# Optimization experiments

Hardware: AMD Instinct MI355X
Metric: run time of the kernel (lower is better)

Reference implementation:

```python
import jax, jax.numpy as jnp
import numpy as np

EMBED_DIM = 1024
NUM_HEADS = 16
HEAD_DIM = EMBED_DIM // NUM_HEADS
SCALE = 1.0 / np.sqrt(HEAD_DIM).astype(np.float32)


def setup_inputs() -> dict:
    key = jax.random.key(0)
    ks = jax.random.split(key, 9)
    B, T, C = 2, 2048, EMBED_DIM
    s = 1.0 / np.sqrt(C).astype(np.float32)  # torch Linear init scale (approx, uniform bound)
    return {
        "x_q": jax.random.normal(ks[0], (B, T, C), dtype=jnp.float32),
        "attn_mask": jnp.zeros((T, T), dtype=jnp.float32),
        "Wq": jax.random.uniform(ks[1], (C, C), jnp.float32, -s, s),
        "bq": jax.random.uniform(ks[2], (C,), jnp.float32, -s, s),
        "Wk": jax.random.uniform(ks[3], (C, C), jnp.float32, -s, s),
        "bk": jax.random.uniform(ks[4], (C,), jnp.float32, -s, s),
        "Wv": jax.random.uniform(ks[5], (C, C), jnp.float32, -s, s),
        "bv": jax.random.uniform(ks[6], (C,), jnp.float32, -s, s),
        "Wo": jax.random.uniform(ks[7], (C, C), jnp.float32, -s, s),
        "bo": jax.random.uniform(ks[8], (C,), jnp.float32, -s, s),
    }


def reference(x_q, attn_mask, Wq, bq, Wk, bk, Wv, bv, Wo, bo):
    B, Tq, C = x_q.shape
    # self-attention: x_kv = x_q
    q = (x_q @ Wq.T + bq).reshape(B, Tq, NUM_HEADS, HEAD_DIM)
    k = (x_q @ Wk.T + bk).reshape(B, Tq, NUM_HEADS, HEAD_DIM)
    v = (x_q @ Wv.T + bv).reshape(B, Tq, NUM_HEADS, HEAD_DIM)
    # (B, H, Tq, Tk)
    scores = jnp.einsum('bqhd,bkhd->bhqk', q, k) * SCALE
    scores = scores + attn_mask[None, None, :, :]  # 2D additive mask path
    attn = jax.nn.softmax(scores, axis=-1)  # dropout p=0.0 -> identity
    out = jnp.einsum('bhqk,bkhd->bqhd', attn, v).reshape(B, Tq, C)
    out = out @ Wo.T + bo
    return out
```

## Files before the change

kernel.cpp:

```cpp
#include <hip/hip_runtime.h>
#include <hip/hip_bf16.h>
#include <stdint.h>

typedef _Float16 f16x8_t __attribute__((ext_vector_type(8)));
typedef _Float16 f16x4_t __attribute__((ext_vector_type(4)));
typedef float    f32x4_t __attribute__((ext_vector_type(4)));
typedef float    f32x16_t __attribute__((ext_vector_type(16)));

#define T_SEQ 2048
#define NH    16
#define HD    64
#define CDIM  1024
#define NTOK  4096
#define QSCALE 0.18033688011112042f
#define LOG2E  1.4426950408889634f

__device__ __forceinline__ void async_ld16(void* lds, const void* g) {
    __builtin_amdgcn_global_load_lds(
        (const __attribute__((address_space(1))) uint32_t*)g,
        (__attribute__((address_space(3))) uint32_t*)lds, 16, 0, 0);
}

__global__ __launch_bounds__(256)
void prep_all(const float* __restrict__ x, const float* __restrict__ Wq,
              const float* __restrict__ Wk, const float* __restrict__ Wv,
              const float* __restrict__ Wo, const float* __restrict__ mask,
              _Float16* __restrict__ xh, _Float16* __restrict__ Wqkvh,
              _Float16* __restrict__ Woh, int* __restrict__ flag)
{
    const int XQ = NTOK * CDIM / 4;
    const int WQ = CDIM * CDIM / 4;
    int i = blockIdx.x * 256 + threadIdx.x;
    if (i < XQ + 4 * WQ) {
        const float* s; _Float16* d; int off;
        if (i < XQ) { s = x; d = xh; off = i; }
        else {
            int j = i - XQ; int w = j >> 18; off = j & (WQ - 1);
            s = (w == 0) ? Wq : (w == 1) ? Wk : (w == 2) ? Wv : Wo;
            d = (w == 3) ? Woh : Wqkvh + (size_t)w * CDIM * CDIM;
        }
        float4 v = ((const float4*)s)[off];
        f16x4_t h = {(_Float16)v.x, (_Float16)v.y, (_Float16)v.z, (_Float16)v.w};
        ((f16x4_t*)d)[off] = h;
    } else {
        int off = i - (XQ + 4 * WQ);
        float4 v = ((const float4*)mask)[off];
        if (v.x != 0.f || v.y != 0.f || v.z != 0.f || v.w != 0.f) atomicOr(flag, 1);
    }
}

template<int MODE>
__global__ __launch_bounds__(256)
void gemm_f16(const _Float16* __restrict__ Ag, const _Float16* __restrict__ Bg,
              const float* __restrict__ b0, const float* __restrict__ b1,
              const float* __restrict__ b2,
              _Float16* __restrict__ Qo, _Float16* __restrict__ Ko,
              _Float16* __restrict__ Vto, float* __restrict__ Fo)
{
    __shared__ _Float16 sA[3][128 * 32];
    __shared__ _Float16 sB[3][128 * 32];
    const int K = CDIM;
    const int tid  = threadIdx.x;
    const int lane = tid & 63, wv = tid >> 6;
    const int wr = wv >> 1, wc = wv & 1;
    const int bid = blockIdx.x;
    const int xcd = bid & 7, L = bid >> 3;
    const int sb = L & 31, st = L >> 5;
    const int rowA0 = (st * 8 + (sb & 7)) * 128;
    const int rowB0 = (xcd * 4 + (sb >> 3)) * 128;
    const int srow = lane >> 2;
    const int scol = (lane & 3) * 8;
    const int fr = lane & 15, fg = lane >> 4;
    f32x4_t acc[4][4] = {};

#define STAGE(buf, kk) do {                                                     \
        _Pragma("unroll")                                                       \
        for (int i_ = 0; i_ < 2; ++i_) {                                        \
            const int eoff = i_ * 2048 + wv * 512;                              \
            const int r_ = i_ * 64 + wv * 16 + srow;                            \
            async_ld16(&sA[buf][eoff], Ag + (size_t)(rowA0 + r_) * K + (kk) + scol); \
            async_ld16(&sB[buf][eoff], Bg + (size_t)(rowB0 + r_) * K + (kk) + scol); \
        } } while (0)

    STAGE(0, 0);
    int cur = 0;
    for (int k0 = 0; k0 < K; k0 += 32) {
        const int nxt = (cur == 2) ? 0 : cur + 1;
        if (k0 + 32 < K) {
            STAGE(nxt, k0 + 32);
            asm volatile("s_waitcnt vmcnt(4)" ::: "memory");
        } else {
            asm volatile("s_waitcnt vmcnt(0)" ::: "memory");
        }
        __builtin_amdgcn_s_barrier();
        __builtin_amdgcn_sched_barrier(0);
        f16x8_t a[4], b[4];
#pragma unroll
        for (int mi = 0; mi < 4; ++mi)
            a[mi] = *(const f16x8_t*)&sA[cur][(wr * 64 + mi * 16 + fr) * 32 + fg * 8];
#pragma unroll
        for (int ni = 0; ni < 4; ++ni)
            b[ni] = *(const f16x8_t*)&sB[cur][(wc * 64 + ni * 16 + fr) * 32 + fg * 8];
#pragma unroll
        for (int mi = 0; mi < 4; ++mi)
#pragma unroll
            for (int ni = 0; ni < 4; ++ni)
                acc[mi][ni] = __builtin_amdgcn_mfma_f32_16x16x32_f16(a[mi], b[ni], acc[mi][ni], 0, 0, 0);
        cur = nxt;
    }
#undef STAGE

    if (MODE == 0) {
        const int which = rowA0 >> 10;
        const float* bp = (which == 0) ? b0 : ((which == 1) ? b1 : b2);
#pragma unroll
        for (int mi = 0; mi < 4; ++mi) {
            const int cc = (rowA0 & 1023) + wr * 64 + mi * 16 + fg * 4;
            const float4 bv = *(const float4*)&bp[cc];
            const int h = cc >> 6, d0 = cc & 63;
#pragma unroll
            for (int ni = 0; ni < 4; ++ni) {
                const int tok = rowB0 + wc * 64 + ni * 16 + fr;
                const int bh = (tok >> 11) * NH + h, tt = tok & (T_SEQ - 1);
                const float v0 = acc[mi][ni][0] + bv.x, v1 = acc[mi][ni][1] + bv.y;
                const float v2 = acc[mi][ni][2] + bv.z, v3 = acc[mi][ni][3] + bv.w;
                if (which == 0) {
                    f16x4_t hq = {(_Float16)(v0 * QSCALE), (_Float16)(v1 * QSCALE),
                                  (_Float16)(v2 * QSCALE), (_Float16)(v3 * QSCALE)};
                    *(f16x4_t*)&Qo[((size_t)bh * T_SEQ + tt) * HD + d0] = hq;
                } else if (which == 1) {
                    f16x4_t hk = {(_Float16)v0, (_Float16)v1, (_Float16)v2, (_Float16)v3};
                    *(f16x4_t*)&Ko[((size_t)bh * 32 + (tt >> 6)) * 4096 +
                                   (d0 >> 3) * 512 + (tt & 63) * 8 + (d0 & 7)] = hk;
                } else {
                    const size_t vb_ = ((size_t)bh * 32 + (tt >> 6)) * 4096 +
                                       (size_t)((tt >> 3) & 7) * 512 + (tt & 7);
                    Vto[vb_ + (d0 + 0) * 8] = (_Float16)v0;
                    Vto[vb_ + (d0 + 1) * 8] = (_Float16)v1;
                    Vto[vb_ + (d0 + 2) * 8] = (_Float16)v2;
                    Vto[vb_ + (d0 + 3) * 8] = (_Float16)v3;
                }
            }
        }
    } else {
#pragma unroll
        for (int mi = 0; mi < 4; ++mi) {
            const int cc = rowA0 + wr * 64 + mi * 16 + fg * 4;
            const float4 bv = *(const float4*)&b0[cc];
#pragma unroll
            for (int ni = 0; ni < 4; ++ni) {
                const int tok = rowB0 + wc * 64 + ni * 16 + fr;
                float4 ov = {acc[mi][ni][0] + bv.x, acc[mi][ni][1] + bv.y,
                             acc[mi][ni][2] + bv.z, acc[mi][ni][3] + bv.w};
                *(float4*)&Fo[(size_t)tok * CDIM + cc] = ov;
            }
        }
    }
}

__global__ __launch_bounds__(256, 2)
void attn_f16(const _Float16* __restrict__ Q, const _Float16* __restrict__ Kc,
              const _Float16* __restrict__ Vc, const float* __restrict__ mask,
              const int* __restrict__ mflag, _Float16* __restrict__ AO)
{
    __shared__ __align__(16) _Float16 sK[3][4096];
    __shared__ __align__(16) _Float16 sV[3][4096];

    const int tid = threadIdx.x;
    const int lane = tid & 63, wv = tid >> 6;
    const int ln = lane & 31, hi = lane >> 5;
    const int bid = blockIdx.x;
    const int xcd = bid & 7, idx = bid >> 3;
    const int bh = xcd * 4 + (idx & 3);
    const int qx = idx >> 2;
    const int b = bh >> 4, h = bh & (NH - 1);
    const int q0 = qx * 128 + wv * 32;
    const _Float16* Qb  = Q  + (size_t)bh * T_SEQ * HD;
    const _Float16* Kbh = Kc + (size_t)bh * (T_SEQ * HD);
    const _Float16* Vbh = Vc + (size_t)bh * (T_SEQ * HD);
    const int soff = tid * 8;

    f16x8_t qf[4];
#pragma unroll
    for (int dc = 0; dc < 4; ++dc)
        qf[dc] = *(const f16x8_t*)&Qb[(size_t)(q0 + ln) * HD + dc * 16 + hi * 8];

    f32x16_t o0 = {}, o1 = {};
    float m_run = -1e30f, l_run = 0.f;
    const int mf = mflag[0];

    async_ld16(&sK[0][soff],        Kbh + soff);
    async_ld16(&sK[0][2048 + soff], Kbh + 2048 + soff);
    async_ld16(&sV[0][soff],        Vbh + soff);
    async_ld16(&sV[0][2048 + soff], Vbh + 2048 + soff);
    int cur = 0;

    for (int t = 0; t < T_SEQ / 64; ++t) {
        const int nxt = (cur == 2) ? 0 : cur + 1;
        if (t + 1 < T_SEQ / 64) {
            const int goff = (t + 1) * 4096;
            async_ld16(&sK[nxt][soff],        Kbh + goff + soff);
            async_ld16(&sK[nxt][2048 + soff], Kbh + goff + 2048 + soff);
            async_ld16(&sV[nxt][soff],        Vbh + goff + soff);
            async_ld16(&sV[nxt][2048 + soff], Vbh + goff + 2048 + soff);
            asm volatile("s_waitcnt vmcnt(4)" ::: "memory");
        } else {
            asm volatile("s_waitcnt vmcnt(0)" ::: "memory");
        }
        __builtin_amdgcn_s_barrier();
        __builtin_amdgcn_sched_barrier(0);

        f32x16_t s0 = {}, s1 = {};
        __builtin_amdgcn_s_setprio(1);
#pragma unroll
        for (int dc = 0; dc < 4; ++dc) {
            f16x8_t kf0 = *(const f16x8_t*)&sK[cur][(2 * dc + hi) * 512 + ln * 8];
            f16x8_t kf1 = *(const f16x8_t*)&sK[cur][(2 * dc + hi) * 512 + (32 + ln) * 8];
            s0 = __builtin_amdgcn_mfma_f32_32x32x16_f16(kf0, qf[dc], s0, 0, 0, 0);
            s1 = __builtin_amdgcn_mfma_f32_32x32x16_f16(kf1, qf[dc], s1, 0, 0, 0);
        }
        __builtin_amdgcn_s_setprio(0);

        if (mf) {
            const float* mrow = mask + (size_t)(q0 + ln) * T_SEQ + t * 64;
#pragma unroll
            for (int r2 = 0; r2 < 16; ++r2) {
                const int row = (r2 & 3) + 8 * (r2 >> 2) + 4 * hi;
                s0[r2] += mrow[row] * LOG2E;
                s1[r2] += mrow[32 + row] * LOG2E;
            }
        }

        float mt[8];
#pragma unroll
        for (int i = 0; i < 8; ++i)
            mt[i] = fmaxf(fmaxf(s0[2 * i], s0[2 * i + 1]), fmaxf(s1[2 * i], s1[2 * i + 1]));
#pragma unroll
        for (int st = 4; st > 0; st >>= 1)
#pragma unroll
            for (int i = 0; i < st; ++i) mt[i] = fmaxf(mt[i], mt[i + st]);
        float tmax = fmaxf(mt[0], __shfl_xor(mt[0], 32, 64));

        if (!__all(tmax <= m_run + 8.0f)) {
            const float mnew = fmaxf(m_run, tmax);
            const float sc = __builtin_amdgcn_exp2f(m_run - mnew);
            m_run = mnew;
            l_run *= sc;
#pragma unroll
            for (int r2 = 0; r2 < 16; ++r2) {
                const int row = (r2 & 3) + 8 * (r2 >> 2) + 4 * hi;
                const float scr = __shfl(sc, row, 64);
                o0[r2] *= scr;
                o1[r2] *= scr;
            }
        }

#pragma unroll
        for (int r2 = 0; r2 < 16; ++r2) {
            s0[r2] = __builtin_amdgcn_exp2f(s0[r2] - m_run);
            s1[r2] = __builtin_amdgcn_exp2f(s1[r2] - m_run);
        }
        float sm[8];
#pragma unroll
        for (int i = 0; i < 8; ++i)
            sm[i] = (s0[2 * i] + s0[2 * i + 1]) + (s1[2 * i] + s1[2 * i + 1]);
#pragma unroll
        for (int st = 4; st > 0; st >>= 1)
#pragma unroll
            for (int i = 0; i < st; ++i) sm[i] += sm[i + st];
        l_run += sm[0] + __shfl_xor(sm[0], 32, 64);

        f16x8_t pa[4];
#pragma unroll
        for (int g = 0; g < 2; ++g) {
            const f32x16_t& sg = g ? s1 : s0;
            uint32_t W[8];
#pragma unroll
            for (int t2 = 0; t2 < 8; ++t2) {
                auto pk = __builtin_amdgcn_cvt_pkrtz(sg[2 * t2], sg[2 * t2 + 1]);
                W[t2] = __builtin_bit_cast(uint32_t, pk);
            }
#pragma unroll
            for (int c2 = 0; c2 < 2; ++c2) {
                uint32_t a0 = W[4 * c2 + 0], a1 = W[4 * c2 + 1];
                uint32_t a2 = W[4 * c2 + 2], a3 = W[4 * c2 + 3];
                asm("v_permlane32_swap_b32 %0, %1" : "+v"(a0), "+v"(a2));
                asm("v_permlane32_swap_b32 %0, %1" : "+v"(a1), "+v"(a3));
                union { uint32_t w[4]; f16x8_t v; } u;
                u.w[0] = a0; u.w[1] = a1; u.w[2] = a2; u.w[3] = a3;
                pa[g * 2 + c2] = u.v;
            }
        }

        __builtin_amdgcn_s_setprio(1);
#pragma unroll
        for (int c = 0; c < 4; ++c) {
            f16x8_t vb0 = *(const f16x8_t*)&sV[cur][(2 * c + hi) * 512 + ln * 8];
            f16x8_t vb1 = *(const f16x8_t*)&sV[cur][(2 * c + hi) * 512 + (32 + ln) * 8];
            o0 = __builtin_amdgcn_mfma_f32_32x32x16_f16(pa[c], vb0, o0, 0, 0, 0);
            o1 = __builtin_amdgcn_mfma_f32_32x32x16_f16(pa[c], vb1, o1, 0, 0, 0);
        }
        __builtin_amdgcn_s_setprio(0);
        cur = nxt;
    }

    const float linv = 1.f / l_run;
#pragma unroll
    for (int r2 = 0; r2 < 16; ++r2) {
        const int row = (r2 & 3) + 8 * (r2 >> 2) + 4 * hi;
        const float inv = __shfl(linv, row, 64);
        const size_t base = (size_t)(b * T_SEQ + q0 + row) * CDIM + h * HD;
        AO[base + ln]      = (_Float16)(o0[r2] * inv);
        AO[base + 32 + ln] = (_Float16)(o1[r2] * inv);
    }
}

extern "C" void kernel_launch(void* const* d_in, const int* in_sizes, int n_in,
                              void* d_out, int out_size, void* d_ws, size_t ws_size,
                              hipStream_t stream) {
    const float* x    = (const float*)d_in[0];
    const float* mask = (const float*)d_in[1];
    const float* Wq   = (const float*)d_in[2];
    const float* bq   = (const float*)d_in[3];
    const float* Wk   = (const float*)d_in[4];
    const float* bk   = (const float*)d_in[5];
    const float* Wv   = (const float*)d_in[6];
    const float* bv   = (const float*)d_in[7];
    const float* Wo   = (const float*)d_in[8];
    const float* bo   = (const float*)d_in[9];
    float* out = (float*)d_out;

    char* ws = (char*)d_ws;
    _Float16* xh    = (_Float16*)(ws);
    _Float16* Wqkvh = (_Float16*)(ws + (8u  << 20));
    _Float16* Woh   = (_Float16*)(ws + (14u << 20));
    _Float16* Qp    = (_Float16*)(ws + (16u << 20));
    _Float16* Kc    = (_Float16*)(ws + (24u << 20));
    _Float16* Vc    = (_Float16*)(ws + (32u << 20));
    int* mflag      = (int*)(ws + (40u << 20));
    _Float16* AO    = xh;

    hipMemsetAsync(mflag, 0, 4, stream);
    prep_all<<<12288, 256, 0, stream>>>(x, Wq, Wk, Wv, Wo, mask, xh, Wqkvh, Woh, mflag);
    gemm_f16<0><<<768, 256, 0, stream>>>(Wqkvh, xh, bq, bk, bv, Qp, Kc, Vc, nullptr);
    attn_f16<<<512, 256, 0, stream>>>(Qp, Kc, Vc, mask, mflag, AO);
    gemm_f16<1><<<256, 256, 0, stream>>>(Woh, AO, bo, nullptr, nullptr,
                                         nullptr, nullptr, nullptr, out);
}
```

Measured before the change: 128.9 us.

## Split attention KV range across two wave groups with LDS merge

The attention kernel now uses 512-thread blocks in which two 4-wave groups each process half of the key/value sequence for the same 128 query rows. Their online-softmax partial results are merged through shared memory at the end. Each group double-buffers its own K/V tiles and synchronises with __syncthreads, replacing the earlier triple-buffered waitcnt scheme. The aim is more waves per CU and shorter per-wave serial loops, at the cost of an extra merge step, block-wide barriers, and the larger LDS footprint limiting occupancy.

Measured after the change: 131.3 us. Within noise of the previous version (+1.8%).

```diff
diff --git a/kernel.cpp b/kernel.cpp
--- a/kernel.cpp
+++ b/kernel.cpp
@@ -158,27 +158,36 @@
     }
 }
 
-__global__ __launch_bounds__(256, 2)
+__global__ __launch_bounds__(512, 4)
 void attn_f16(const _Float16* __restrict__ Q, const _Float16* __restrict__ Kc,
               const _Float16* __restrict__ Vc, const float* __restrict__ mask,
               const int* __restrict__ mflag, _Float16* __restrict__ AO)
 {
-    __shared__ __align__(16) _Float16 sK[3][4096];
-    __shared__ __align__(16) _Float16 sV[3][4096];
+    __shared__ __align__(16) _Float16 smem[32768];
 
     const int tid = threadIdx.x;
     const int lane = tid & 63, wv = tid >> 6;
+    const int g = wv >> 2, wl = wv & 3;
     const int ln = lane & 31, hi = lane >> 5;
     const int bid = blockIdx.x;
-    const int xcd = bid & 7, idx = bid >> 3;
-    const int bh = xcd * 4 + (idx & 3);
-    const int qx = idx >> 2;
+    const int swz = (bid & 7) * 64 + (bid >> 3);
+    const int qx = swz & 15, bh = swz >> 4;
     const int b = bh >> 4, h = bh & (NH - 1);
-    const int q0 = qx * 128 + wv * 32;
+    const int q0 = qx * 128 + wl * 32;
     const _Float16* Qb  = Q  + (size_t)bh * T_SEQ * HD;
     const _Float16* Kbh = Kc + (size_t)bh * (T_SEQ * HD);
     const _Float16* Vbh = Vc + (size_t)bh * (T_SEQ * HD);
-    const int soff = tid * 8;
+    _Float16* pK = smem + g * 16384;
+    _Float16* pV = pK + 8192;
+    const int soff = (tid & 255) * 8;
+
+#define ASTAGE(buf, t) do {                                                   \
+        const int goff_ = (t) * 4096;                                         \
+        async_ld16(&pK[(buf) * 4096 + soff],        Kbh + goff_ + soff);        \
+        async_ld16(&pK[(buf) * 4096 + 2048 + soff], Kbh + goff_ + 2048 + soff); \
+        async_ld16(&pV[(buf) * 4096 + soff],        Vbh + goff_ + soff);        \
+        async_ld16(&pV[(buf) * 4096 + 2048 + soff], Vbh + goff_ + 2048 + soff); \
+    } while (0)
 
     f16x8_t qf[4];
 #pragma unroll
@@ -188,34 +197,22 @@
     f32x16_t o0 = {}, o1 = {};
     float m_run = -1e30f, l_run = 0.f;
     const int mf = mflag[0];
-
-    async_ld16(&sK[0][soff],        Kbh + soff);
-    async_ld16(&sK[0][2048 + soff], Kbh + 2048 + soff);
-    async_ld16(&sV[0][soff],        Vbh + soff);
-    async_ld16(&sV[0][2048 + soff], Vbh + 2048 + soff);
+    const int tbase = g * 16;
+
+    ASTAGE(0, tbase);
     int cur = 0;
 
-    for (int t = 0; t < T_SEQ / 64; ++t) {
-        const int nxt = (cur == 2) ? 0 : cur + 1;
-        if (t + 1 < T_SEQ / 64) {
-            const int goff = (t + 1) * 4096;
-            async_ld16(&sK[nxt][soff],        Kbh + goff + soff);
-            async_ld16(&sK[nxt][2048 + soff], Kbh + goff + 2048 + soff);
-            async_ld16(&sV[nxt][soff],        Vbh + goff + soff);
-            async_ld16(&sV[nxt][2048 + soff], Vbh + goff + 2048 + soff);
-            asm volatile("s_waitcnt vmcnt(4)" ::: "memory");
-        } else {
-            asm volatile("s_waitcnt vmcnt(0)" ::: "memory");
-        }
-        __builtin_amdgcn_s_barrier();
-        __builtin_amdgcn_sched_barrier(0);
+    for (int i = 0; i < 16; ++i) {
+        const int t = tbase + i;
+        __syncthreads();
+        if (i + 1 < 16) ASTAGE(cur ^ 1, t + 1);
 
         f32x16_t s0 = {}, s1 = {};
         __builtin_amdgcn_s_setprio(1);
 #pragma unroll
         for (int dc = 0; dc < 4; ++dc) {
-            f16x8_t kf0 = *(const f16x8_t*)&sK[cur][(2 * dc + hi) * 512 + ln * 8];
-            f16x8_t kf1 = *(const f16x8_t*)&sK[cur][(2 * dc + hi) * 512 + (32 + ln) * 8];
+            f16x8_t kf0 = *(const f16x8_t*)&pK[cur * 4096 + (2 * dc + hi) * 512 + ln * 8];
+            f16x8_t kf1 = *(const f16x8_t*)&pK[cur * 4096 + (2 * dc + hi) * 512 + (32 + ln) * 8];
             s0 = __builtin_amdgcn_mfma_f32_32x32x16_f16(kf0, qf[dc], s0, 0, 0, 0);
             s1 = __builtin_amdgcn_mfma_f32_32x32x16_f16(kf1, qf[dc], s1, 0, 0, 0);
         }
@@ -233,12 +230,12 @@
 
         float mt[8];
 #pragma unroll
-        for (int i = 0; i < 8; ++i)
-            mt[i] = fmaxf(fmaxf(s0[2 * i], s0[2 * i + 1]), fmaxf(s1[2 * i], s1[2 * i + 1]));
+        for (int i2 = 0; i2 < 8; ++i2)
+            mt[i2] = fmaxf(fmaxf(s0[2 * i2], s0[2 * i2 + 1]), fmaxf(s1[2 * i2], s1[2 * i2 + 1]));
 #pragma unroll
         for (int st = 4; st > 0; st >>= 1)
 #pragma unroll
-            for (int i = 0; i < st; ++i) mt[i] = fmaxf(mt[i], mt[i + st]);
+            for (int i2 = 0; i2 < st; ++i2) mt[i2] = fmaxf(mt[i2], mt[i2 + st]);
         float tmax = fmaxf(mt[0], __shfl_xor(mt[0], 32, 64));
 
         if (!__all(tmax <= m_run + 8.0f)) {
@@ -262,18 +259,18 @@
         }
         float sm[8];
 #pragma unroll
-        for (int i = 0; i < 8; ++i)
-            sm[i] = (s0[2 * i] + s0[2 * i + 1]) + (s1[2 * i] + s1[2 * i + 1]);
+        for (int i2 = 0; i2 < 8; ++i2)
+            sm[i2] = (s0[2 * i2] + s0[2 * i2 + 1]) + (s1[2 * i2] + s1[2 * i2 + 1]);
 #pragma unroll
         for (int st = 4; st > 0; st >>= 1)
 #pragma unroll
-            for (int i = 0; i < st; ++i) sm[i] += sm[i + st];
+            for (int i2 = 0; i2 < st; ++i2) sm[i2] += sm[i2 + st];
         l_run += sm[0] + __shfl_xor(sm[0], 32, 64);
 
         f16x8_t pa[4];
 #pragma unroll
-        for (int g = 0; g < 2; ++g) {
-            const f32x16_t& sg = g ? s1 : s0;
+        for (int gg = 0; gg < 2; ++gg) {
+            const f32x16_t& sg = gg ? s1 : s0;
             uint32_t W[8];
 #pragma unroll
             for (int t2 = 0; t2 < 8; ++t2) {
@@ -288,31 +285,54 @@
                 asm("v_permlane32_swap_b32 %0, %1" : "+v"(a1), "+v"(a3));
                 union { uint32_t w[4]; f16x8_t v; } u;
                 u.w[0] = a0; u.w[1] = a1; u.w[2] = a2; u.w[3] = a3;
-                pa[g * 2 + c2] = u.v;
+                pa[gg * 2 + c2] = u.v;
             }
         }
 
         __builtin_amdgcn_s_setprio(1);
 #pragma unroll
         for (int c = 0; c < 4; ++c) {
-            f16x8_t vb0 = *(const f16x8_t*)&sV[cur][(2 * c + hi) * 512 + ln * 8];
-            f16x8_t vb1 = *(const f16x8_t*)&sV[cur][(2 * c + hi) * 512 + (32 + ln) * 8];
+            f16x8_t vb0 = *(const f16x8_t*)&pV[cur * 4096 + (2 * c + hi) * 512 + ln * 8];
+            f16x8_t vb1 = *(const f16x8_t*)&pV[cur * 4096 + (2 * c + hi) * 512 + (32 + ln) * 8];
             o0 = __builtin_amdgcn_mfma_f32_32x32x16_f16(pa[c], vb0, o0, 0, 0, 0);
             o1 = __builtin_amdgcn_mfma_f32_32x32x16_f16(pa[c], vb1, o1, 0, 0, 0);
         }
         __builtin_amdgcn_s_setprio(0);
-        cur = nxt;
-    }
-
-    const float linv = 1.f / l_run;
-#pragma unroll
-    for (int r2 = 0; r2 < 16; ++r2) {
-        const int row = (r2 & 3) + 8 * (r2 >> 2) + 4 * hi;
-        const float inv = __shfl(linv, row, 64);
-        const size_t base = (size_t)(b * T_SEQ + q0 + row) * CDIM + h * HD;
-        AO[base + ln]      = (_Float16)(o0[r2] * inv);
-        AO[base + 32 + ln] = (_Float16)(o1[r2] * inv);
-    }
+        cur ^= 1;
+    }
+
+    __syncthreads();
+    float* mrg = (float*)smem;
+    const int mbase = (wl * 64 + lane) * 34;
+    if (g == 1) {
+        mrg[mbase]     = m_run;
+        mrg[mbase + 1] = l_run;
+#pragma unroll
+        for (int r2 = 0; r2 < 16; ++r2) {
+            mrg[mbase + 2 + r2]  = o0[r2];
+            mrg[mbase + 18 + r2] = o1[r2];
+        }
+    }
+    __syncthreads();
+    if (g == 0) {
+        const float m1 = mrg[mbase];
+        const float l1 = mrg[mbase + 1];
+        const float mm  = fmaxf(m_run, m1);
+        const float sc0 = __builtin_amdgcn_exp2f(m_run - mm);
+        const float sc1 = __builtin_amdgcn_exp2f(m1 - mm);
+        const float linv = 1.f / (l_run * sc0 + l1 * sc1);
+#pragma unroll
+        for (int r2 = 0; r2 < 16; ++r2) {
+            const int row = (r2 & 3) + 8 * (r2 >> 2) + 4 * hi;
+            const float s0r = __shfl(sc0, row, 64);
+            const float s1r = __shfl(sc1, row, 64);
+            const float ir  = __shfl(linv, row, 64);
+            const size_t base = (size_t)(b * T_SEQ + q0 + row) * CDIM + h * HD;
+            AO[base + ln]      = (_Float16)((o0[r2] * s0r + mrg[mbase + 2 + r2]  * s1r) * ir);
+            AO[base + 32 + ln] = (_Float16)((o1[r2] * s0r + mrg[mbase + 18 + r2] * s1r) * ir);
+        }
+    }
+#undef ASTAGE
 }
 
 extern "C" void kernel_launch(void* const* d_in, const int* in_sizes, int n_in,
@@ -343,7 +363,7 @@
     hipMemsetAsync(mflag, 0, 4, stream);
     prep_all<<<12288, 256, 0, stream>>>(x, Wq, Wk, Wv, Wo, mask, xh, Wqkvh, Woh, mflag);
     gemm_f16<0><<<768, 256, 0, stream>>>(Wqkvh, xh, bq, bk, bv, Qp, Kc, Vc, nullptr);
-    attn_f16<<<512, 256, 0, stream>>>(Qp, Kc, Vc, mask, mflag, AO);
+    attn_f16<<<512, 512, 0, stream>>>(Qp, Kc, Vc, mask, mflag, AO);
     gemm_f16<1><<<256, 256, 0, stream>>>(Woh, AO, bo, nullptr, nullptr,
                                          nullptr, nullptr, nullptr, out);
 }
```
